# Kernel tuning notes

Hardware: AMD Instinct MI355X
Metric: run time of the kernel (lower is better)

The kernel has to match this reference:

```python
import jax, jax.numpy as jnp
import numpy as np

_LOG2PI = float(np.log(2.0 * np.pi))


def setup_inputs() -> dict:
    key = jax.random.key(0)
    ks = jax.random.split(key, 9)
    B, T, S, A, O = 64, 128, 512, 16, 4096
    regime = jax.random.randint(ks[0], (B,), 0, 2).astype(jnp.float32)
    obs = jax.random.randint(ks[1], (T + 1, B), 0, O, dtype=jnp.int32)
    rewards = jax.random.normal(ks[2], (T + 1, B), jnp.float32)
    dones = jnp.zeros((T + 1, B), jnp.float32)
    actions = jax.random.randint(ks[3], (T, B), 0, A, dtype=jnp.int32)
    prior_logits = jax.random.normal(ks[4], (S,), jnp.float32)
    trans_logits = jax.random.normal(ks[5], (A, S, S), jnp.float32)
    obs_logits = jax.random.normal(ks[6], (S, O), jnp.float32)
    policy_logits = jax.random.normal(ks[7], (S, A), jnp.float32)
    r_mu = jax.random.normal(ks[8], (S,), jnp.float32)
    r_logsig = jnp.zeros((S,), jnp.float32)
    return {"regime": regime, "obs": obs, "rewards": rewards, "dones": dones,
            "actions": actions, "prior_logits": prior_logits,
            "trans_logits": trans_logits, "obs_logits": obs_logits,
            "policy_logits": policy_logits, "r_mu": r_mu, "r_logsig": r_logsig}


def _log_prob(regime, obs, rewards, dones, actions, prior_logits, trans_logits,
              obs_logits, policy_logits, r_mu, r_logsig):
    # normalized log-prob tables (tabular instantiation of AugmentedModel)
    log_prior = jax.nn.log_softmax(prior_logits)              # [S]
    log_trans = jax.nn.log_softmax(trans_logits, axis=-1)     # [A,S,S]
    log_obs = jax.nn.log_softmax(obs_logits, axis=-1)         # [S,O]
    log_pol = jax.nn.log_softmax(policy_logits, axis=-1)      # [S,A]
    lse = jax.scipy.special.logsumexp

    def emis(o, r):  # log q(o|s) + log q(r|s) -> [B,S]
        lo = log_obs.T[o]                                      # [B,S] gather
        lr = (-0.5 * (((r[:, None] - r_mu[None, :]) * jnp.exp(-r_logsig)[None, :]) ** 2)
              - r_logsig[None, :] - 0.5 * _LOG2PI)             # [B,S]
        return lo + lr

    def act_term(a, done):  # masked log q(a|s) -> [B,S]
        la = log_pol.T[a]                                      # [B,S]
        la = jnp.where((done == 1.0)[:, None], jnp.zeros_like(la), la)
        la = jnp.where((regime == 1.0)[:, None], jnp.zeros_like(la), la)
        return la

    T = actions.shape[0]
    B = regime.shape[0]

    # t = 0
    was_done = jnp.zeros((B,), rewards.dtype)
    done0 = dones[0]
    lq_sorda = log_prior[None, :] + emis(obs[0], rewards[0]) + act_term(actions[0], done0)
    lq_orda = lse(lq_sorda, axis=-1) * (1.0 - was_done)        # [B]
    log_prob = lq_orda
    lq_s_h = lq_sorda - lq_orda[:, None]
    # belief propagation through transition: [B,S,1] + [B,S,S] -> lse over prev state
    lq_snext_h = lse(lq_s_h[:, :, None] + log_trans[actions[0]], axis=1)

    def step(carry, xs):  # t = 1 .. T-1 (has an action)
        log_prob, was_done, lq_s_hprev = carry
        o, r, d, a = xs
        done = jnp.maximum(was_done, d)
        lq = lq_s_hprev + emis(o, r) + act_term(a, done)
        lq_orda = lse(lq, axis=-1) * (1.0 - was_done)
        log_prob = jnp.where(jnp.isinf(log_prob), log_prob, log_prob + lq_orda)
        lq_s_h = lq - lq_orda[:, None]
        lq_snext = lse(lq_s_h[:, :, None] + log_trans[a], axis=1)
        return (log_prob, done, lq_snext), None

    xs = (obs[1:T], rewards[1:T], dones[1:T], actions[1:T])
    (log_prob, was_done, lq_s_hprev), _ = jax.lax.scan(
        step, (log_prob, done0, lq_snext_h), xs)

    # final step t = T (no action term)
    lq = lq_s_hprev + emis(obs[T], rewards[T])
    lq_ord = lse(lq, axis=-1) * (1.0 - was_done)
    log_prob = jnp.where(jnp.isinf(log_prob), log_prob, log_prob + lq_ord)
    return log_prob


def reference(regime, obs, rewards, dones, actions, prior_logits, trans_logits,
              obs_logits, policy_logits, r_mu, r_logsig):
    return _log_prob(regime, obs, rewards, dones, actions, prior_logits,
                     trans_logits, obs_logits, policy_logits, r_mu, r_logsig)
```

## Files before the change

kernel.cpp:

```cpp
#include <hip/hip_runtime.h>
#include <math.h>

#define DI __device__ __forceinline__

constexpr int BB = 64;
constexpr int TT = 128;
constexpr int SS = 512;
constexpr int AA = 16;
constexpr int OO = 4096;
constexpr float LOG2PI = 1.8378770664093453f;
constexpr float LOG4096 = 8.317766166719343f;

typedef float f32x4 __attribute__((ext_vector_type(4)));

DI void lds_barrier() {
    asm volatile("s_waitcnt lgkmcnt(0)\n\ts_barrier" ::: "memory");
}

DI unsigned int f32_to_e4m3(float x) {
    unsigned int u = __float_as_uint(x);
    unsigned int lsb = (u >> 20) & 1u;
    unsigned int rounded = u + 0x7ffffu + lsb;
    int e8 = (int)(rounded >> 23) - 120;
    unsigned int m3 = (rounded >> 20) & 7u;
    unsigned int norm = ((unsigned int)e8 << 3) | m3;
    int sub = __float2int_rn(x * 512.0f);
    return (e8 <= 0) ? (unsigned int)sub : norm;
}

DI float bflyMax(float v) {
#pragma unroll
    for (int off = 32; off; off >>= 1) v = fmaxf(v, __shfl_xor(v, off));
    return v;
}
DI float bflySum(float v) {
#pragma unroll
    for (int off = 32; off; off >>= 1) v += __shfl_xor(v, off);
    return v;
}
DI float halfMax(float v) {
#pragma unroll
    for (int off = 16; off; off >>= 1) v = fmaxf(v, __shfl_xor(v, off));
    return v;
}
DI float halfSum(float v) {
#pragma unroll
    for (int off = 16; off; off >>= 1) v += __shfl_xor(v, off);
    return v;
}

template <int NW>
DI float blockMax(float v, float* wr) {
    v = bflyMax(v);
    const int lane = threadIdx.x & 63, wv = threadIdx.x >> 6;
    if (lane == 0) wr[wv] = v;
    __syncthreads();
    float r = wr[0];
#pragma unroll
    for (int i = 1; i < NW; ++i) r = fmaxf(r, wr[i]);
    __syncthreads();
    return r;
}
template <int NW>
DI float blockSum(float v, float* wr) {
    v = bflySum(v);
    const int lane = threadIdx.x & 63, wv = threadIdx.x >> 6;
    if (lane == 0) wr[wv] = v;
    __syncthreads();
    float r = wr[0];
#pragma unroll
    for (int i = 1; i < NW; ++i) r += wr[i];
    __syncthreads();
    return r;
}


__global__ __launch_bounds__(1024) void k_pack(const float* __restrict__ tl,
                                               unsigned char* __restrict__ PB) {
    __shared__ unsigned char lds[16384];
    const int a = blockIdx.x >> 4;
    const int kt = blockIdx.x & 15;
    const int tid = threadIdx.x;
    const int r = tid >> 5;
    const int nt = tid & 31;
    const int k = kt * 32 + r;
    const float* row = tl + ((size_t)a * SS + k) * SS + nt * 16;

    float x[16];
#pragma unroll
    for (int i = 0; i < 4; ++i) {
        float4 v = ((const float4*)row)[i];
        x[4 * i] = v.x; x[4 * i + 1] = v.y; x[4 * i + 2] = v.z; x[4 * i + 3] = v.w;
    }
    float mx = -INFINITY;
#pragma unroll
    for (int i = 0; i < 16; ++i) mx = fmaxf(mx, x[i]);
    mx = halfMax(mx);
    float e[16];
    float sm = 0.f;
#pragma unroll
    for (int i = 0; i < 16; ++i) { e[i] = __expf(x[i] - mx); sm += e[i]; }
    sm = halfSum(sm);
    const float scale = 256.0f / sm;

    const int base = (nt >> 1) * 1024 + ((r >> 3) * 16) * 16 + (nt & 1) * 8 + (r & 7);
#pragma unroll
    for (int i = 0; i < 16; ++i) {
        lds[base + i * 16] = (unsigned char)f32_to_e4m3(e[i] * scale);
    }
    __syncthreads();

    ulonglong2* dst = (ulonglong2*)(PB + (size_t)(a * 16 + kt) * 16384);
    dst[tid] = ((const ulonglong2*)lds)[tid];
}

__global__ __launch_bounds__(256) void k_obs_stats(const float* __restrict__ ol,
                                                   float* __restrict__ mo,
                                                   float* __restrict__ lo) {
    __shared__ float wr[4];
    const int s = blockIdx.x;
    const float* in = ol + (size_t)s * OO;
    const int tid = threadIdx.x;
    float mx = -INFINITY;
    for (int i = tid; i < OO; i += 256) mx = fmaxf(mx, in[i]);
    float m = blockMax<4>(mx, wr);
    float sm = 0.f;
    for (int i = tid; i < OO; i += 256) sm += __expf(in[i] - m);
    float sum = blockSum<4>(sm, wr);
    if (tid == 0) { mo[s] = m; lo[s] = __logf(sum); }
}

__global__ __launch_bounds__(256) void k_obsT(const float* __restrict__ ol,
                                              const float* __restrict__ mo,
                                              const float* __restrict__ lo,
                                              float* __restrict__ obsT) {
    __shared__ float tile[64][65];
    const int tO = blockIdx.x % (OO / 64);
    const int tS = blockIdx.x / (OO / 64);
    const int o0 = tO * 64, s0 = tS * 64;
    const int cc = threadIdx.x & 63, rr = threadIdx.x >> 6;
#pragma unroll
    for (int j = 0; j < 16; ++j) {
        int r = rr + j * 4;
        tile[r][cc] = ol[(size_t)(s0 + r) * OO + o0 + cc] - mo[s0 + r] - lo[s0 + r];
    }
    __syncthreads();
#pragma unroll
    for (int j = 0; j < 16; ++j) {
        int r = rr + j * 4;
        obsT[(size_t)(o0 + r) * SS + s0 + cc] = tile[cc][r];
    }
}

__global__ __launch_bounds__(512, 2) void k_main(
    const float* __restrict__ regime, const int* __restrict__ obs,
    const float* __restrict__ rewards, const float* __restrict__ dones,
    const int* __restrict__ actions, const float* __restrict__ prior_logits,
    const unsigned char* __restrict__ PB, const float* __restrict__ obsT,
    const float* __restrict__ policy_logits, const float* __restrict__ r_mu,
    const float* __restrict__ r_logsig, float* __restrict__ out) {
    __shared__ float wrm[8], wrs[8];
    __shared__ unsigned char p8[4 * 144 + 16];
    __shared__ int obs_l[TT + 1];
    __shared__ float rew_l[TT + 1];
    __shared__ float done_l[TT + 1];
    __shared__ int act_l[TT];

    const int b = blockIdx.x;
    const int tid = threadIdx.x;
    const int wv = tid >> 6, lane = tid & 63, quad = lane >> 4;
    const int s = tid;
    const int wvl16 = wv * 2048 + lane * 16;
    const int p8idx = ((s >> 3) & 3) * 144 + (s >> 5) * 8 + (s & 7);

    if (tid <= TT) {
        obs_l[tid] = obs[tid * BB + b];
        rew_l[tid] = rewards[tid * BB + b];
        done_l[tid] = dones[tid * BB + b];
        if (tid < TT) act_l[tid] = actions[tid * BB + b];
    }
    float la16[16];
    {
        const float4* pr4 = (const float4*)(policy_logits + (size_t)s * AA);
        float4 v0 = pr4[0], v1 = pr4[1], v2 = pr4[2], v3 = pr4[3];
        la16[0] = v0.x; la16[1] = v0.y; la16[2] = v0.z; la16[3] = v0.w;
        la16[4] = v1.x; la16[5] = v1.y; la16[6] = v1.z; la16[7] = v1.w;
        la16[8] = v2.x; la16[9] = v2.y; la16[10] = v2.z; la16[11] = v2.w;
        la16[12] = v3.x; la16[13] = v3.y; la16[14] = v3.z; la16[15] = v3.w;
        float mx = la16[0];
#pragma unroll
        for (int i = 1; i < 16; ++i) mx = fmaxf(mx, la16[i]);
        float sm = 0.f;
#pragma unroll
        for (int i = 0; i < 16; ++i) sm += __expf(la16[i] - mx);
        float ls = mx + __logf(sm);
#pragma unroll
        for (int i = 0; i < 16; ++i) la16[i] -= ls;
    }
    const float rm = r_mu[s];
    const float rls = r_logsig[s];
    const float inv_sig = __expf(-rls);
    const float reg = regime[b];

    float px = prior_logits[s];
    {
        float wm0 = bflyMax(px);
        if (lane == 0) wrm[wv] = wm0;
    }
    lds_barrier();
    float pm = wrm[0];
#pragma unroll
    for (int i = 1; i < 8; ++i) pm = fmaxf(pm, wrm[i]);
    {
        float ws0 = bflySum(__expf(px - pm));
        if (lane == 0) wrs[wv] = ws0;
    }
    lds_barrier();
    float psum = wrs[0];
#pragma unroll
    for (int i = 1; i < 8; ++i) psum += wrs[i];
    float base_reg = px - pm - __logf(psum);

    ulonglong2 fA[8], fB[8], gA[8], gB[8];
    {
        const int a0 = __builtin_amdgcn_readfirstlane(act_l[0]);
        const unsigned char* P0 = PB + (size_t)a0 * (16 * 16384) + wvl16;
#pragma unroll
        for (int c = 0; c < 8; ++c) {
            fA[c] = *(const ulonglong2*)(P0 + c * 16384);
            fB[c] = *(const ulonglong2*)(P0 + c * 16384 + 1024);
        }
    }
    float obsv = obsT[(size_t)obs_l[0] * SS + s];

    float log_prob = 0.f;
    float was_done = 0.f;

#define CHUNK_L(c, CA, CB)                                                      \
    {                                                                           \
        long af = *(const long long*)(p8 + quad * 144 + (c) * 8);               \
        acc0 = __builtin_amdgcn_mfma_f32_16x16x32_fp8_fp8((long)CA[(c)].x, af, acc0, 0, 0, 0); \
        acc1 = __builtin_amdgcn_mfma_f32_16x16x32_fp8_fp8((long)CA[(c)].y, af, acc1, 0, 0, 0); \
        acc2 = __builtin_amdgcn_mfma_f32_16x16x32_fp8_fp8((long)CB[(c)].x, af, acc2, 0, 0, 0); \
        acc3 = __builtin_amdgcn_mfma_f32_16x16x32_fp8_fp8((long)CB[(c)].y, af, acc3, 0, 0, 0); \
        CA[(c)] = *(const ulonglong2*)(Pw_ + ((c) + 8) * 16384);                \
        CB[(c)] = *(const ulonglong2*)(Pw_ + ((c) + 8) * 16384 + 1024);         \
    }
#define CHUNK_H(c, CA, CB, NA, NB)                                              \
    {                                                                           \
        long af = *(const long long*)(p8 + quad * 144 + (c) * 8);               \
        acc0 = __builtin_amdgcn_mfma_f32_16x16x32_fp8_fp8((long)CA[(c) - 8].x, af, acc0, 0, 0, 0); \
        acc1 = __builtin_amdgcn_mfma_f32_16x16x32_fp8_fp8((long)CA[(c) - 8].y, af, acc1, 0, 0, 0); \
        acc2 = __builtin_amdgcn_mfma_f32_16x16x32_fp8_fp8((long)CB[(c) - 8].x, af, acc2, 0, 0, 0); \
        acc3 = __builtin_amdgcn_mfma_f32_16x16x32_fp8_fp8((long)CB[(c) - 8].y, af, acc3, 0, 0, 0); \
        NA[(c) - 8] = *(const ulonglong2*)(Pn_ + ((c) - 8) * 16384);            \
        NB[(c) - 8] = *(const ulonglong2*)(Pn_ + ((c) - 8) * 16384 + 1024);     \
    }

#define STEP(T, CA, CB, NA, NB)                                                 \
    {                                                                           \
        const int t_ = (T);                                                     \
        const float r_ = rew_l[t_];                                             \
        const int a_ = __builtin_amdgcn_readfirstlane(act_l[t_]);               \
        const float d_ = done_l[t_];                                            \
        const float done_ = fmaxf(was_done, d_);                                \
        const unsigned char* Pw_ = PB + (size_t)a_ * (16 * 16384) + wvl16;      \
        const int tn_ = (t_ + 1 < TT) ? t_ + 1 : 0;                             \
        const int an_ = __builtin_amdgcn_readfirstlane(act_l[tn_]);             \
        const unsigned char* Pn_ = PB + (size_t)an_ * (16 * 16384) + wvl16;     \
        float obsv_next_ = obsT[(size_t)obs_l[t_ + 1] * SS + s];                \
                \
        float diff_ = (r_ - rm) * inv_sig;                                      \
        float emis_ = obsv - 0.5f * diff_ * diff_ - rls - 0.5f * LOG2PI;        \
        float la_ = la16[0];                                                    \
        _Pragma("unroll")                                                       \
        for (int i = 1; i < 16; ++i) la_ = (a_ == i) ? la16[i] : la_;           \
        if (done_ == 1.0f || reg == 1.0f) la_ = 0.f;                            \
        float lq_ = base_reg + emis_ + la_;                                     \
        float wmax_ = bflyMax(lq_);                                             \
        if (lane == 0) wrm[wv] = wmax_;                                         \
        lds_barrier();                                                  \
        float m_ = wrm[0];                                                      \
        _Pragma("unroll")                                                       \
        for (int i = 1; i < 8; ++i) m_ = fmaxf(m_, wrm[i]);                     \
        float exv_ = __expf(lq_ - m_);                                          \
        p8[p8idx] = (unsigned char)f32_to_e4m3(exv_ * 16.0f);                   \
        float wsum_ = bflySum(exv_);                                            \
        if (lane == 0) wrs[wv] = wsum_;                                         \
        lds_barrier();                                   \
        float sum_ = wrs[0];                                                    \
        _Pragma("unroll")                                                       \
        for (int i = 1; i < 8; ++i) sum_ += wrs[i];                             \
        float lse_ = m_ + __logf(sum_);                                         \
        float lqo_ = lse_ * (1.0f - was_done);                                  \
        if (!isinf(log_prob)) log_prob += lqo_;                                 \
        was_done = done_;                                                       \
        \
        const float basev_ = m_ - lqo_ - LOG4096;                               \
        f32x4 acc0 = {0.f, 0.f, 0.f, 0.f};                                      \
        f32x4 acc1 = {0.f, 0.f, 0.f, 0.f};                                      \
        f32x4 acc2 = {0.f, 0.f, 0.f, 0.f};                                      \
        f32x4 acc3 = {0.f, 0.f, 0.f, 0.f};                                      \
        CHUNK_L(0, CA, CB)  CHUNK_L(1, CA, CB)  CHUNK_L(2, CA, CB)              \
        CHUNK_L(3, CA, CB)  CHUNK_L(4, CA, CB)  CHUNK_L(5, CA, CB)              \
        CHUNK_L(6, CA, CB)  CHUNK_L(7, CA, CB)                                  \
        CHUNK_H(8, CA, CB, NA, NB)   CHUNK_H(9, CA, CB, NA, NB)                 \
        CHUNK_H(10, CA, CB, NA, NB)  CHUNK_H(11, CA, CB, NA, NB)                \
        CHUNK_H(12, CA, CB, NA, NB)  CHUNK_H(13, CA, CB, NA, NB)                \
        CHUNK_H(14, CA, CB, NA, NB)  CHUNK_H(15, CA, CB, NA, NB)                \
           \
        float t0_ = __shfl(acc0[0], lane & 15);                                 \
        float t1_ = __shfl(acc1[0], lane & 15);                                 \
        float t2_ = __shfl(acc2[0], lane & 15);                                 \
        float t3_ = __shfl(acc3[0], lane & 15);                                 \
        float av_ = quad == 0 ? t0_ : (quad == 1 ? t1_ : (quad == 2 ? t2_ : t3_)); \
        base_reg = basev_ + __logf(av_);                                        \
        obsv = obsv_next_;                                                      \
        asm volatile("" ::: "memory");      \
    }

    for (int t = 0; t < TT; t += 2) {
        STEP(t, fA, fB, gA, gB)
        STEP(t + 1, gA, gB, fA, fB)
    }
#undef STEP
#undef CHUNK_L
#undef CHUNK_H

    {
        const float r = rew_l[TT];
        float diff = (r - rm) * inv_sig;
        float emis = obsv - 0.5f * diff * diff - rls - 0.5f * LOG2PI;
        float lq = base_reg + emis;
        float wmax = bflyMax(lq);
        if (lane == 0) wrm[wv] = wmax;
        lds_barrier();
        float m = wrm[0];
#pragma unroll
        for (int i = 1; i < 8; ++i) m = fmaxf(m, wrm[i]);
        float wsum = bflySum(__expf(lq - m));
        if (lane == 0) wrs[wv] = wsum;
        lds_barrier();
        float sum = wrs[0];
#pragma unroll
        for (int i = 1; i < 8; ++i) sum += wrs[i];
        float lse = m + __logf(sum);
        float lq_ord = lse * (1.0f - was_done);
        if (!isinf(log_prob)) log_prob += lq_ord;
    }

    if (tid == 0) out[b] = log_prob;
}

extern "C" void kernel_launch(void* const* d_in, const int* in_sizes, int n_in,
                              void* d_out, int out_size, void* d_ws, size_t ws_size,
                              hipStream_t stream) {
    const float* regime = (const float*)d_in[0];
    const int* obs = (const int*)d_in[1];
    const float* rewards = (const float*)d_in[2];
    const float* dones = (const float*)d_in[3];
    const int* actions = (const int*)d_in[4];
    const float* prior_logits = (const float*)d_in[5];
    const float* trans_logits = (const float*)d_in[6];
    const float* obs_logits = (const float*)d_in[7];
    const float* policy_logits = (const float*)d_in[8];
    const float* r_mu = (const float*)d_in[9];
    const float* r_logsig = (const float*)d_in[10];
    float* out = (float*)d_out;

    char* ws = (char*)d_ws;
    unsigned char* PB = (unsigned char*)ws;
    float* obsT = (float*)(ws + (size_t)AA * SS * SS);
    float* mo = (float*)(ws + (size_t)AA * SS * SS + (size_t)OO * SS * 4);
    float* lo = mo + SS;

    k_pack<<<256, 1024, 0, stream>>>(trans_logits, PB);
    k_obs_stats<<<SS, 256, 0, stream>>>(obs_logits, mo, lo);
    k_obsT<<<(OO / 64) * (SS / 64), 256, 0, stream>>>(obs_logits, mo, lo, obsT);
    k_main<<<BB, 512, 0, stream>>>(regime, obs, rewards, dones, actions, prior_logits,
                                   PB, obsT, policy_logits, r_mu, r_logsig, out);
}
```

Baseline: 476.8 us.

## Split each batch recurrence across two workgroups exchanging partial state via global mailboxes

Each batch element's forward recurrence is now handled by two blocks, each owning half of the 512 states. The blocks exchange fp8-packed probability slices, the running max and the partial sum through a global mailbox guarded by an agent-scope release/acquire flag. Each block then runs only half the MFMA work on its own columns and merges the two partial log-sum-exps. The aim is to double the number of CUs working on the sequential scan and halve each block's per-step matrix work. The cost is a cross-block spin-wait every timestep, and it relies on both blocks being co-resident to avoid deadlock.

```diff
diff --git a/kernel.cpp b/kernel.cpp
--- a/kernel.cpp
+++ b/kernel.cpp
@@ -158,20 +158,31 @@
     const int* __restrict__ actions, const float* __restrict__ prior_logits,
     const unsigned char* __restrict__ PB, const float* __restrict__ obsT,
     const float* __restrict__ policy_logits, const float* __restrict__ r_mu,
-    const float* __restrict__ r_logsig, float* __restrict__ out) {
+    const float* __restrict__ r_logsig, unsigned int* __restrict__ flags,
+    char* __restrict__ mbox, float* __restrict__ out) {
     __shared__ float wrm[8], wrs[8];
-    __shared__ unsigned char p8[4 * 144 + 16];
+    __shared__ float xsc[2];
+    __shared__ alignas(16) unsigned char p8[4 * 144 + 16];
+    __shared__ float plds[SS];
     __shared__ int obs_l[TT + 1];
     __shared__ float rew_l[TT + 1];
     __shared__ float done_l[TT + 1];
     __shared__ int act_l[TT];
 
-    const int b = blockIdx.x;
+    const int bid = blockIdx.x;
+    const int h = bid >> 6;
+    const int b = bid & 63;
     const int tid = threadIdx.x;
     const int wv = tid >> 6, lane = tid & 63, quad = lane >> 4;
-    const int s = tid;
-    const int wvl16 = wv * 2048 + lane * 16;
-    const int p8idx = ((s >> 3) & 3) * 144 + (s >> 5) * 8 + (s & 7);
+    const int KOWN = 8 * h;
+    const int KOTH = 8 * (1 - h);
+    const int sg = 256 * h + 32 * wv + (lane & 31);
+    const int woff = (8 * h + wv) * 1024 + lane * 16;
+
+    unsigned int* flagW = flags + (size_t)(b * 2 + h) * 16;
+    unsigned int* flagR = flags + (size_t)(b * 2 + (1 - h)) * 16;
+    char* mboxW = mbox + (size_t)(b * 2 + h) * 1024;
+    const char* mboxR = mbox + (size_t)(b * 2 + (1 - h)) * 1024;
 
     if (tid <= TT) {
         obs_l[tid] = obs[tid * BB + b];
@@ -181,7 +192,7 @@
     }
     float la16[16];
     {
-        const float4* pr4 = (const float4*)(policy_logits + (size_t)s * AA);
+        const float4* pr4 = (const float4*)(policy_logits + (size_t)sg * AA);
         float4 v0 = pr4[0], v1 = pr4[1], v2 = pr4[2], v3 = pr4[3];
         la16[0] = v0.x; la16[1] = v0.y; la16[2] = v0.z; la16[3] = v0.w;
         la16[4] = v1.x; la16[5] = v1.y; la16[6] = v1.z; la16[7] = v1.w;
@@ -197,79 +208,74 @@
 #pragma unroll
         for (int i = 0; i < 16; ++i) la16[i] -= ls;
     }
-    const float rm = r_mu[s];
-    const float rls = r_logsig[s];
+    const float rm = r_mu[sg];
+    const float rls = r_logsig[sg];
     const float inv_sig = __expf(-rls);
     const float reg = regime[b];
 
-    float px = prior_logits[s];
     {
+        float px = prior_logits[tid];
         float wm0 = bflyMax(px);
         if (lane == 0) wrm[wv] = wm0;
-    }
-    lds_barrier();
-    float pm = wrm[0];
-#pragma unroll
-    for (int i = 1; i < 8; ++i) pm = fmaxf(pm, wrm[i]);
-    {
+        lds_barrier();
+        float pm = wrm[0];
+#pragma unroll
+        for (int i = 1; i < 8; ++i) pm = fmaxf(pm, wrm[i]);
         float ws0 = bflySum(__expf(px - pm));
         if (lane == 0) wrs[wv] = ws0;
+        lds_barrier();
+        float psum = wrs[0];
+#pragma unroll
+        for (int i = 1; i < 8; ++i) psum += wrs[i];
+        plds[tid] = px - pm - __logf(psum);
     }
     lds_barrier();
-    float psum = wrs[0];
-#pragma unroll
-    for (int i = 1; i < 8; ++i) psum += wrs[i];
-    float base_reg = px - pm - __logf(psum);
-
-    ulonglong2 fA[8], fB[8], gA[8], gB[8];
+    float base_reg = plds[sg];
+
+    ulonglong2 fO[8], fP[8], gO[8], gP[8];
     {
         const int a0 = __builtin_amdgcn_readfirstlane(act_l[0]);
-        const unsigned char* P0 = PB + (size_t)a0 * (16 * 16384) + wvl16;
+        const unsigned char* P0 = PB + (size_t)a0 * (16 * 16384) + woff;
 #pragma unroll
         for (int c = 0; c < 8; ++c) {
-            fA[c] = *(const ulonglong2*)(P0 + c * 16384);
-            fB[c] = *(const ulonglong2*)(P0 + c * 16384 + 1024);
+            fO[c] = *(const ulonglong2*)(P0 + (size_t)(KOWN + c) * 16384);
+            fP[c] = *(const ulonglong2*)(P0 + (size_t)(KOTH + c) * 16384);
         }
     }
-    float obsv = obsT[(size_t)obs_l[0] * SS + s];
+    float obsv = obsT[(size_t)obs_l[0] * SS + sg];
 
     float log_prob = 0.f;
     float was_done = 0.f;
 
-#define CHUNK_L(c, CA, CB)                                                      \
+#define OWNC(c, CO, NO)                                                         \
     {                                                                           \
-        long af = *(const long long*)(p8 + quad * 144 + (c) * 8);               \
-        acc0 = __builtin_amdgcn_mfma_f32_16x16x32_fp8_fp8((long)CA[(c)].x, af, acc0, 0, 0, 0); \
-        acc1 = __builtin_amdgcn_mfma_f32_16x16x32_fp8_fp8((long)CA[(c)].y, af, acc1, 0, 0, 0); \
-        acc2 = __builtin_amdgcn_mfma_f32_16x16x32_fp8_fp8((long)CB[(c)].x, af, acc2, 0, 0, 0); \
-        acc3 = __builtin_amdgcn_mfma_f32_16x16x32_fp8_fp8((long)CB[(c)].y, af, acc3, 0, 0, 0); \
-        CA[(c)] = *(const ulonglong2*)(Pw_ + ((c) + 8) * 16384);                \
-        CB[(c)] = *(const ulonglong2*)(Pw_ + ((c) + 8) * 16384 + 1024);         \
-    }
-#define CHUNK_H(c, CA, CB, NA, NB)                                              \
+        long af = *(const long long*)(p8 + quad * 144 + (KOWN + (c)) * 8);      \
+        accO0 = __builtin_amdgcn_mfma_f32_16x16x32_fp8_fp8((long)CO[(c)].x, af, accO0, 0, 0, 0); \
+        accO1 = __builtin_amdgcn_mfma_f32_16x16x32_fp8_fp8((long)CO[(c)].y, af, accO1, 0, 0, 0); \
+        NO[(c)] = *(const ulonglong2*)(Pn_ + (size_t)(KOWN + (c)) * 16384);     \
+    }
+#define OTHC(c, CP, NP)                                                         \
     {                                                                           \
-        long af = *(const long long*)(p8 + quad * 144 + (c) * 8);               \
-        acc0 = __builtin_amdgcn_mfma_f32_16x16x32_fp8_fp8((long)CA[(c) - 8].x, af, acc0, 0, 0, 0); \
-        acc1 = __builtin_amdgcn_mfma_f32_16x16x32_fp8_fp8((long)CA[(c) - 8].y, af, acc1, 0, 0, 0); \
-        acc2 = __builtin_amdgcn_mfma_f32_16x16x32_fp8_fp8((long)CB[(c) - 8].x, af, acc2, 0, 0, 0); \
-        acc3 = __builtin_amdgcn_mfma_f32_16x16x32_fp8_fp8((long)CB[(c) - 8].y, af, acc3, 0, 0, 0); \
-        NA[(c) - 8] = *(const ulonglong2*)(Pn_ + ((c) - 8) * 16384);            \
-        NB[(c) - 8] = *(const ulonglong2*)(Pn_ + ((c) - 8) * 16384 + 1024);     \
-    }
-
-#define STEP(T, CA, CB, NA, NB)                                                 \
+        long af = *(const long long*)(p8 + quad * 144 + (KOTH + (c)) * 8);      \
+        accP0 = __builtin_amdgcn_mfma_f32_16x16x32_fp8_fp8((long)CP[(c)].x, af, accP0, 0, 0, 0); \
+        accP1 = __builtin_amdgcn_mfma_f32_16x16x32_fp8_fp8((long)CP[(c)].y, af, accP1, 0, 0, 0); \
+        NP[(c)] = *(const ulonglong2*)(Pn_ + (size_t)(KOTH + (c)) * 16384);     \
+    }
+
+#define STEP(T, CO, CP, NO, NP)                                                 \
     {                                                                           \
         const int t_ = (T);                                                     \
         const float r_ = rew_l[t_];                                             \
         const int a_ = __builtin_amdgcn_readfirstlane(act_l[t_]);               \
         const float d_ = done_l[t_];                                            \
         const float done_ = fmaxf(was_done, d_);                                \
-        const unsigned char* Pw_ = PB + (size_t)a_ * (16 * 16384) + wvl16;      \
         const int tn_ = (t_ + 1 < TT) ? t_ + 1 : 0;                             \
         const int an_ = __builtin_amdgcn_readfirstlane(act_l[tn_]);             \
-        const unsigned char* Pn_ = PB + (size_t)an_ * (16 * 16384) + wvl16;     \
-        float obsv_next_ = obsT[(size_t)obs_l[t_ + 1] * SS + s];                \
-                \
+        const unsigned char* Pn_ = PB + (size_t)an_ * (16 * 16384) + woff;      \
+        char* pw_ = mboxW + (t_ & 1) * 512;                                     \
+        const char* pr_ = mboxR + (t_ & 1) * 512;                               \
+        float obsv_next_ = obsT[(size_t)obs_l[t_ + 1] * SS + sg];               \
+                                                         \
         float diff_ = (r_ - rm) * inv_sig;                                      \
         float emis_ = obsv - 0.5f * diff_ * diff_ - rls - 0.5f * LOG2PI;        \
         float la_ = la16[0];                                                    \
@@ -277,79 +283,154 @@
         for (int i = 1; i < 16; ++i) la_ = (a_ == i) ? la16[i] : la_;           \
         if (done_ == 1.0f || reg == 1.0f) la_ = 0.f;                            \
         float lq_ = base_reg + emis_ + la_;                                     \
-        float wmax_ = bflyMax(lq_);                                             \
+        float wmax_ = halfMax(lq_);                                             \
         if (lane == 0) wrm[wv] = wmax_;                                         \
         lds_barrier();                                                  \
-        float m_ = wrm[0];                                                      \
+        float mA_ = wrm[0];                                                     \
         _Pragma("unroll")                                                       \
-        for (int i = 1; i < 8; ++i) m_ = fmaxf(m_, wrm[i]);                     \
-        float exv_ = __expf(lq_ - m_);                                          \
-        p8[p8idx] = (unsigned char)f32_to_e4m3(exv_ * 16.0f);                   \
-        float wsum_ = bflySum(exv_);                                            \
+        for (int i = 1; i < 8; ++i) mA_ = fmaxf(mA_, wrm[i]);                   \
+        float exv_ = __expf(lq_ - mA_);                                         \
+        if (lane < 32)                                                          \
+            p8[(lane >> 3) * 144 + (KOWN + wv) * 8 + (lane & 7)] =              \
+                (unsigned char)f32_to_e4m3(exv_ * 16.0f);                       \
+        float wsum_ = halfSum(exv_);                                            \
         if (lane == 0) wrs[wv] = wsum_;                                         \
-        lds_barrier();                                   \
-        float sum_ = wrs[0];                                                    \
+        lds_barrier();                     \
+        float sumA_ = wrs[0];                                                   \
         _Pragma("unroll")                                                       \
-        for (int i = 1; i < 8; ++i) sum_ += wrs[i];                             \
+        for (int i = 1; i < 8; ++i) sumA_ += wrs[i];                            \
+                                                        \
+        if (wv == 6) {                                           \
+            if (lane < 32) {                                                    \
+                unsigned long long v_ = *(const unsigned long long*)(           \
+                    p8 + (lane >> 3) * 144 + (KOWN + (lane & 7)) * 8);          \
+                __hip_atomic_store((unsigned long long*)(pw_ + lane * 8), v_,   \
+                                   __ATOMIC_RELAXED, __HIP_MEMORY_SCOPE_AGENT); \
+            } else if (lane == 32) {                                            \
+                __hip_atomic_store((unsigned int*)(pw_ + 256),                  \
+                                   __float_as_uint(mA_),                        \
+                                   __ATOMIC_RELAXED, __HIP_MEMORY_SCOPE_AGENT); \
+            } else if (lane == 33) {                                            \
+                __hip_atomic_store((unsigned int*)(pw_ + 260),                  \
+                                   __float_as_uint(sumA_),                      \
+                                   __ATOMIC_RELAXED, __HIP_MEMORY_SCOPE_AGENT); \
+            }                                                                   \
+            if (lane == 0)                                                      \
+                __hip_atomic_store(flagW, (unsigned)(t_ + 1),                   \
+                                   __ATOMIC_RELEASE, __HIP_MEMORY_SCOPE_AGENT); \
+        }                                                                       \
+        if (wv == 7) {                                            \
+            while (__hip_atomic_load(flagR, __ATOMIC_ACQUIRE,                   \
+                                     __HIP_MEMORY_SCOPE_AGENT) <                \
+                   (unsigned)(t_ + 1))                                          \
+                __builtin_amdgcn_s_sleep(1);                                    \
+            if (lane < 32) {                                                    \
+                unsigned long long v_ = __hip_atomic_load(                      \
+                    (const unsigned long long*)(pr_ + lane * 8),                \
+                    __ATOMIC_RELAXED, __HIP_MEMORY_SCOPE_AGENT);                \
+                *(unsigned long long*)(p8 + (lane >> 3) * 144 +                 \
+                                       (KOTH + (lane & 7)) * 8) = v_;           \
+            } else if (lane == 32) {                                            \
+                xsc[0] = __uint_as_float(__hip_atomic_load(                     \
+                    (const unsigned int*)(pr_ + 256),                           \
+                    __ATOMIC_RELAXED, __HIP_MEMORY_SCOPE_AGENT));               \
+            } else if (lane == 33) {                                            \
+                xsc[1] = __uint_as_float(__hip_atomic_load(                     \
+                    (const unsigned int*)(pr_ + 260),                           \
+                    __ATOMIC_RELAXED, __HIP_MEMORY_SCOPE_AGENT));               \
+            }                                                                   \
+        }                                                                       \
+                    \
+        f32x4 accO0 = {0.f, 0.f, 0.f, 0.f};                                     \
+        f32x4 accO1 = {0.f, 0.f, 0.f, 0.f};                                     \
+        f32x4 accP0 = {0.f, 0.f, 0.f, 0.f};                                     \
+        f32x4 accP1 = {0.f, 0.f, 0.f, 0.f};                                     \
+        OWNC(0, CO, NO) OWNC(1, CO, NO) OWNC(2, CO, NO) OWNC(3, CO, NO)         \
+        OWNC(4, CO, NO) OWNC(5, CO, NO) OWNC(6, CO, NO) OWNC(7, CO, NO)         \
+        lds_barrier();                 \
+        float mB_ = xsc[0];                                                     \
+        float sumB_ = xsc[1];                                                   \
+        OTHC(0, CP, NP) OTHC(1, CP, NP) OTHC(2, CP, NP) OTHC(3, CP, NP)         \
+        OTHC(4, CP, NP) OTHC(5, CP, NP) OTHC(6, CP, NP) OTHC(7, CP, NP)         \
+        float m_ = fmaxf(mA_, mB_);                                             \
+        float sO_ = __expf(mA_ - m_);                                           \
+        float sP_ = __expf(mB_ - m_);                                           \
+        float sum_ = sO_ * sumA_ + sP_ * sumB_;                                 \
         float lse_ = m_ + __logf(sum_);                                         \
         float lqo_ = lse_ * (1.0f - was_done);                                  \
         if (!isinf(log_prob)) log_prob += lqo_;                                 \
         was_done = done_;                                                       \
-        \
-        const float basev_ = m_ - lqo_ - LOG4096;                               \
-        f32x4 acc0 = {0.f, 0.f, 0.f, 0.f};                                      \
-        f32x4 acc1 = {0.f, 0.f, 0.f, 0.f};                                      \
-        f32x4 acc2 = {0.f, 0.f, 0.f, 0.f};                                      \
-        f32x4 acc3 = {0.f, 0.f, 0.f, 0.f};                                      \
-        CHUNK_L(0, CA, CB)  CHUNK_L(1, CA, CB)  CHUNK_L(2, CA, CB)              \
-        CHUNK_L(3, CA, CB)  CHUNK_L(4, CA, CB)  CHUNK_L(5, CA, CB)              \
-        CHUNK_L(6, CA, CB)  CHUNK_L(7, CA, CB)                                  \
-        CHUNK_H(8, CA, CB, NA, NB)   CHUNK_H(9, CA, CB, NA, NB)                 \
-        CHUNK_H(10, CA, CB, NA, NB)  CHUNK_H(11, CA, CB, NA, NB)                \
-        CHUNK_H(12, CA, CB, NA, NB)  CHUNK_H(13, CA, CB, NA, NB)                \
-        CHUNK_H(14, CA, CB, NA, NB)  CHUNK_H(15, CA, CB, NA, NB)                \
-           \
-        float t0_ = __shfl(acc0[0], lane & 15);                                 \
-        float t1_ = __shfl(acc1[0], lane & 15);                                 \
-        float t2_ = __shfl(acc2[0], lane & 15);                                 \
-        float t3_ = __shfl(acc3[0], lane & 15);                                 \
-        float av_ = quad == 0 ? t0_ : (quad == 1 ? t1_ : (quad == 2 ? t2_ : t3_)); \
-        base_reg = basev_ + __logf(av_);                                        \
+        float av0_ = sO_ * accO0[0] + sP_ * accP0[0];                           \
+        float av1_ = sO_ * accO1[0] + sP_ * accP1[0];                           \
+        float g0_ = __shfl(av0_, lane & 15);                                    \
+        float g1_ = __shfl(av1_, lane & 15);                                    \
+        float av_ = ((lane & 31) < 16) ? g0_ : g1_;                             \
+        base_reg = m_ - lqo_ - LOG4096 + __logf(av_);                           \
         obsv = obsv_next_;                                                      \
-        asm volatile("" ::: "memory");      \
+        asm volatile("" ::: "memory");     \
     }
 
     for (int t = 0; t < TT; t += 2) {
-        STEP(t, fA, fB, gA, gB)
-        STEP(t + 1, gA, gB, fA, fB)
+        STEP(t, fO, fP, gO, gP)
+        STEP(t + 1, gO, gP, fO, fP)
     }
 #undef STEP
-#undef CHUNK_L
-#undef CHUNK_H
+#undef OWNC
+#undef OTHC
 
     {
         const float r = rew_l[TT];
         float diff = (r - rm) * inv_sig;
         float emis = obsv - 0.5f * diff * diff - rls - 0.5f * LOG2PI;
         float lq = base_reg + emis;
-        float wmax = bflyMax(lq);
+        float wmax = halfMax(lq);
         if (lane == 0) wrm[wv] = wmax;
         lds_barrier();
-        float m = wrm[0];
-#pragma unroll
-        for (int i = 1; i < 8; ++i) m = fmaxf(m, wrm[i]);
-        float wsum = bflySum(__expf(lq - m));
+        float mA = wrm[0];
+#pragma unroll
+        for (int i = 1; i < 8; ++i) mA = fmaxf(mA, wrm[i]);
+        float wsum = halfSum(__expf(lq - mA));
         if (lane == 0) wrs[wv] = wsum;
         lds_barrier();
-        float sum = wrs[0];
-#pragma unroll
-        for (int i = 1; i < 8; ++i) sum += wrs[i];
+        float sumA = wrs[0];
+#pragma unroll
+        for (int i = 1; i < 8; ++i) sumA += wrs[i];
+        char* pw_ = mboxW + (TT & 1) * 512;
+        const char* pr_ = mboxR + (TT & 1) * 512;
+        if (wv == 6) {
+            if (lane == 32)
+                __hip_atomic_store((unsigned int*)(pw_ + 256), __float_as_uint(mA),
+                                   __ATOMIC_RELAXED, __HIP_MEMORY_SCOPE_AGENT);
+            else if (lane == 33)
+                __hip_atomic_store((unsigned int*)(pw_ + 260), __float_as_uint(sumA),
+                                   __ATOMIC_RELAXED, __HIP_MEMORY_SCOPE_AGENT);
+            if (lane == 0)
+                __hip_atomic_store(flagW, (unsigned)(TT + 1),
+                                   __ATOMIC_RELEASE, __HIP_MEMORY_SCOPE_AGENT);
+        }
+        if (wv == 7) {
+            while (__hip_atomic_load(flagR, __ATOMIC_ACQUIRE,
+                                     __HIP_MEMORY_SCOPE_AGENT) < (unsigned)(TT + 1))
+                __builtin_amdgcn_s_sleep(1);
+            if (lane == 32)
+                xsc[0] = __uint_as_float(__hip_atomic_load(
+                    (const unsigned int*)(pr_ + 256),
+                    __ATOMIC_RELAXED, __HIP_MEMORY_SCOPE_AGENT));
+            else if (lane == 33)
+                xsc[1] = __uint_as_float(__hip_atomic_load(
+                    (const unsigned int*)(pr_ + 260),
+                    __ATOMIC_RELAXED, __HIP_MEMORY_SCOPE_AGENT));
+        }
+        lds_barrier();
+        float mB = xsc[0], sumB = xsc[1];
+        float m = fmaxf(mA, mB);
+        float sum = __expf(mA - m) * sumA + __expf(mB - m) * sumB;
         float lse = m + __logf(sum);
         float lq_ord = lse * (1.0f - was_done);
         if (!isinf(log_prob)) log_prob += lq_ord;
     }
 
-    if (tid == 0) out[b] = log_prob;
+    if (h == 0 && tid == 0) out[b] = log_prob;
 }
 
 extern "C" void kernel_launch(void* const* d_in, const int* in_sizes, int n_in,
@@ -371,12 +452,17 @@
     char* ws = (char*)d_ws;
     unsigned char* PB = (unsigned char*)ws;
     float* obsT = (float*)(ws + (size_t)AA * SS * SS);
-    float* mo = (float*)(ws + (size_t)AA * SS * SS + (size_t)OO * SS * 4);
+    size_t tail = (size_t)AA * SS * SS + (size_t)OO * SS * 4;
+    float* mo = (float*)(ws + tail);
     float* lo = mo + SS;
-
+    unsigned int* flags = (unsigned int*)(ws + tail + 16384);
+    char* mbox = (char*)(ws + tail + 16384 + 8192);
+
+    hipMemsetAsync(flags, 0, 128 * 64, stream);
     k_pack<<<256, 1024, 0, stream>>>(trans_logits, PB);
     k_obs_stats<<<SS, 256, 0, stream>>>(obs_logits, mo, lo);
     k_obsT<<<(OO / 64) * (SS / 64), 256, 0, stream>>>(obs_logits, mo, lo, obsT);
-    k_main<<<BB, 512, 0, stream>>>(regime, obs, rewards, dones, actions, prior_logits,
-                                   PB, obsT, policy_logits, r_mu, r_logsig, out);
-}
+    k_main<<<2 * BB, 512, 0, stream>>>(regime, obs, rewards, dones, actions,
+                                       prior_logits, PB, obsT, policy_logits,
+                                       r_mu, r_logsig, flags, mbox, out);
+}
```

Measured after the change: 861.6 us. 1.81x slower.
